# Kernel tuning notes

Hardware: AMD Instinct MI355X
Metric: run time of the kernel (lower is better)

Reference implementation:

```python
import jax, jax.numpy as jnp
import numpy as np

B, N, K = 8, 2048, 30
NF, EF = 128, 128
NPE, NRBF, MAXREL = 16, 16, 32


def _normalize(x, axis=-1, eps=1e-8):
    return x / (jnp.linalg.norm(x, axis=axis, keepdims=True) + eps)


def _gather_nodes(feat, idx):
    # feat [B,N,C], idx [B,N,K] -> [B,N,K,C]
    b = jnp.arange(feat.shape[0])[:, None, None]
    return feat[b, idx]


def _layernorm(x, g, b, eps=1e-5):
    mu = jnp.mean(x, -1, keepdims=True)
    var = jnp.var(x, -1, keepdims=True)
    return (x - mu) * jax.lax.rsqrt(var + eps) * g + b


def _dihedrals(X, eps=1e-7):
    # X [B,N,4,3]; use N,CA,C atoms -> [B,N,6] cos/sin of phi/psi/omega
    Bb, Nn = X.shape[0], X.shape[1]
    Xb = X[:, :, :3, :].reshape(Bb, 3 * Nn, 3)
    U = _normalize(Xb[:, 1:] - Xb[:, :-1])
    u2, u1, u0 = U[:, :-2], U[:, 1:-1], U[:, 2:]
    n2 = _normalize(jnp.cross(u2, u1))
    n1 = _normalize(jnp.cross(u1, u0))
    cosD = jnp.clip(jnp.sum(n2 * n1, -1), -1.0 + eps, 1.0 - eps)
    D = jnp.sign(jnp.sum(u2 * n1, -1)) * jnp.arccos(cosD)
    D = jnp.pad(D, ((0, 0), (1, 2))).reshape(Bb, Nn, 3)
    return jnp.concatenate([jnp.cos(D), jnp.sin(D)], -1)


def _quaternions(R):
    # R [B,N,K,3,3] -> unit quaternion [B,N,K,4]
    Rxx, Ryy, Rzz = R[..., 0, 0], R[..., 1, 1], R[..., 2, 2]
    mag = 0.5 * jnp.sqrt(jnp.abs(1.0 + jnp.stack(
        [Rxx - Ryy - Rzz, -Rxx + Ryy - Rzz, -Rxx - Ryy + Rzz], -1)))
    signs = jnp.sign(jnp.stack(
        [R[..., 2, 1] - R[..., 1, 2], R[..., 0, 2] - R[..., 2, 0], R[..., 1, 0] - R[..., 0, 1]], -1))
    xyz = signs * mag
    w = 0.5 * jnp.sqrt(jax.nn.relu(1.0 + Rxx + Ryy + Rzz))[..., None]
    return _normalize(jnp.concatenate([xyz, w], -1))


def _orientations_coarse(Ca, E_idx):
    # local backbone frames + neighbor direction (3) and relative quaternion (4)
    Bb, Nn = Ca.shape[0], Ca.shape[1]
    U = _normalize(Ca[:, 1:] - Ca[:, :-1])
    u2, u1 = U[:, :-2], U[:, 1:-1]
    n2 = _normalize(jnp.cross(u2, u1))
    o1 = _normalize(u2 - u1)
    O = jnp.stack([o1, n2, jnp.cross(o1, n2)], 2).reshape(Bb, Nn - 3, 9)
    O = jnp.pad(O, ((0, 0), (1, 2), (0, 0)))  # [B,N,9]
    O_nb = _gather_nodes(O, E_idx).reshape(Bb, Nn, -1, 3, 3)
    X_nb = _gather_nodes(Ca, E_idx)
    Of = O.reshape(Bb, Nn, 3, 3)
    dX = X_nb - Ca[:, :, None, :]
    dU = _normalize(jnp.einsum('bnij,bnkj->bnki', Of, dX))
    R = jnp.einsum('bnji,bnkjl->bnkil', Of, O_nb)  # O_i^T @ O_j
    Q = _quaternions(R)
    return jnp.concatenate([dU, Q], -1)  # [B,N,K,7]


def _rbf(D):
    mu = jnp.linspace(2.0, 22.0, NRBF)
    sigma = (22.0 - 2.0) / NRBF
    return jnp.exp(-(((D[..., None] - mu) / sigma) ** 2))


def setup_inputs() -> dict:
    key = jax.random.key(0)
    ks = jax.random.split(key, 8)
    X = jax.random.normal(ks[0], (B, N, 4, 3), dtype=jnp.float32)
    mask = jnp.ones((B, N), dtype=jnp.float32)
    residue_idx = jnp.arange(B * N, dtype=jnp.int32).reshape(B, N)
    chain_labels = jnp.zeros((B, N), dtype=jnp.int32)
    d_pe_in = 2 * MAXREL + 2  # 66
    e_in = NPE + NRBF + 7     # 39
    p = {
        'pe_w': jax.random.normal(ks[1], (d_pe_in, NPE)) / np.sqrt(d_pe_in),
        'pe_b': jnp.zeros((NPE,)),
        'node_l_w': jax.random.normal(ks[2], (6, NF)) / np.sqrt(6.0),
        'node_l_b': jnp.zeros((NF,)),
        'node_emb_w': jax.random.normal(ks[3], (NF, NF)) / np.sqrt(NF),
        'node_emb_b': jnp.zeros((NF,)),
        'edge_l_w': jax.random.normal(ks[4], (e_in, EF)) / np.sqrt(e_in),
        'edge_l_b': jnp.zeros((EF,)),
        'edge_emb_w': jax.random.normal(ks[5], (EF, EF)) / np.sqrt(EF),
        'edge_emb_b': jnp.zeros((EF,)),
        'nn_g': jnp.ones((NF,)), 'nn_b': jnp.zeros((NF,)),
        'ne_g': jnp.ones((EF,)), 'ne_b': jnp.zeros((EF,)),
    }
    return dict(X=X, mask=mask, residue_idx=residue_idx, chain_labels=chain_labels, **p)


def reference(X, mask, residue_idx, chain_labels, pe_w, pe_b, node_l_w, node_l_b,
              node_emb_w, node_emb_b, edge_l_w, edge_l_b, edge_emb_w, edge_emb_b,
              nn_g, nn_b, ne_g, ne_b):
    Ca = X[:, :, 1, :]
    mask2 = mask[:, :, None] * mask[:, None, :]
    D = jnp.sqrt(jnp.sum((Ca[:, :, None] - Ca[:, None, :]) ** 2, -1) + 1e-6)
    D_adj = D + (1.0 - mask2) * 10000.0
    negD, E_idx = jax.lax.top_k(-D_adj, K)  # k nearest
    D_nb = -negD                            # [B,N,K]
    RBF = _rbf(D_nb)                        # [B,N,K,16]
    O_feat = _orientations_coarse(Ca, E_idx)  # [B,N,K,7]
    # positional encodings on gathered residue offsets, masked by chain identity
    offset = residue_idx[:, :, None] - residue_idx[:, None, :]
    off_nb = jnp.take_along_axis(offset, E_idx, axis=2)
    chain_eq = (chain_labels[:, :, None] == chain_labels[:, None, :]).astype(jnp.int32)
    ch_nb = jnp.take_along_axis(chain_eq, E_idx, axis=2)
    d = jnp.clip(off_nb + MAXREL, 0, 2 * MAXREL) * ch_nb + (1 - ch_nb) * (2 * MAXREL + 1)
    d1h = jax.nn.one_hot(d, 2 * MAXREL + 2, dtype=jnp.float32)
    E_pos = d1h @ pe_w + pe_b               # [B,N,K,16]
    V = _dihedrals(X)                       # [B,N,6]
    E = jnp.concatenate([E_pos, RBF, O_feat], -1)  # [B,N,K,39]
    hV = (V @ node_l_w + node_l_b) @ node_emb_w + node_emb_b
    V_out = _layernorm(hV, nn_g, nn_b)
    hE = (E @ edge_l_w + edge_l_b) @ edge_emb_w + edge_emb_b
    E_out = _layernorm(hE, ne_g, ne_b)
    return V_out, E_out, E_idx
```

## Files before the change

kernel.cpp:

```cpp
#include <hip/hip_runtime.h>
#include <hip/hip_bf16.h>
#include <math.h>

#define BB 8
#define NN 2048
#define KK 30
#define NF 128
#define EF 128
#define NPE 16
#define NRBF 16
#define MAXREL 32

#define V_OUT_SZ   (BB*NN*NF)
#define E_OUT_OFF  (V_OUT_SZ)
#define E_OUT_SZ   (BB*NN*KK*EF)
#define EIDX_OUT_OFF (E_OUT_OFF + E_OUT_SZ)

#define WS_EIDX_OFF 0
#define WS_DNB_OFF  1966080
#define WS_O_OFF    3932160
#define WS_V6_OFF   4521984
#define WS_CA4_OFF  4915200
#define WS_W1_OFF   5177344
#define WS_W2_OFF   5193728

typedef __attribute__((ext_vector_type(8))) short bf16x8;
typedef __attribute__((ext_vector_type(4))) float f32x4;
#define MFMA16(a,b,c) __builtin_amdgcn_mfma_f32_16x16x32_bf16(a,b,c,0,0,0)

struct F3 { float x, y, z; };
__device__ inline F3 f3sub(F3 a, F3 b){ return {a.x-b.x, a.y-b.y, a.z-b.z}; }
__device__ inline F3 f3cross(F3 a, F3 b){ return {a.y*b.z - a.z*b.y, a.z*b.x - a.x*b.z, a.x*b.y - a.y*b.x}; }
__device__ inline float f3dot(F3 a, F3 b){ return a.x*b.x + a.y*b.y + a.z*b.z; }
__device__ inline F3 f3norm(F3 v){
    float n = sqrtf(f3dot(v, v));
    float r = 1.0f/(n + 1e-8f);
    return {v.x*r, v.y*r, v.z*r};
}
__device__ inline float sgnf(float x){ return (x>0.f)?1.f:((x<0.f)?-1.f:0.f); }
__device__ inline short f2bf(float f){
    union { __hip_bfloat16 h; short s; } u;
    u.h = __float2bfloat16(f);
    return u.s;
}

template<int CTRL>
__device__ __forceinline__ float fmin_dpp(float x){
    int xi = __float_as_int(x);
    int yi = __builtin_amdgcn_update_dpp(xi, xi, CTRL, 0xf, 0xf, false);
    return fminf(x, __int_as_float(yi));
}
template<int CTRL>
__device__ __forceinline__ unsigned umin_dpp(unsigned x){
    int yi = __builtin_amdgcn_update_dpp((int)x, (int)x, CTRL, 0xf, 0xf, false);
    return min(x, (unsigned)yi);
}

#if __has_builtin(__builtin_amdgcn_permlane16_swap)
__device__ __forceinline__ float fmin_x16(float x){
    unsigned xb = __float_as_uint(x);
    auto r = __builtin_amdgcn_permlane16_swap(xb, xb, false, false);
    return fminf(x, fminf(__uint_as_float(r[0]), __uint_as_float(r[1])));
}
__device__ __forceinline__ unsigned umin_x16(unsigned x){
    auto r = __builtin_amdgcn_permlane16_swap(x, x, false, false);
    return min(x, min((unsigned)r[0], (unsigned)r[1]));
}
#else
__device__ __forceinline__ float fmin_x16(float x){
    int yi = __builtin_amdgcn_ds_swizzle(__float_as_int(x), 0x401F);
    return fminf(x, __int_as_float(yi));
}
__device__ __forceinline__ unsigned umin_x16(unsigned x){
    int yi = __builtin_amdgcn_ds_swizzle((int)x, 0x401F);
    return min(x, (unsigned)yi);
}
#endif

#if __has_builtin(__builtin_amdgcn_permlane32_swap)
__device__ __forceinline__ float fmin_x32(float x){
    unsigned xb = __float_as_uint(x);
    auto r = __builtin_amdgcn_permlane32_swap(xb, xb, false, false);
    return fminf(x, fminf(__uint_as_float(r[0]), __uint_as_float(r[1])));
}
__device__ __forceinline__ unsigned umin_x32(unsigned x){
    auto r = __builtin_amdgcn_permlane32_swap(x, x, false, false);
    return min(x, min((unsigned)r[0], (unsigned)r[1]));
}
#else
__device__ __forceinline__ float fmin_x32(float x){
    return fminf(x, __shfl_xor(x, 32, 64));
}
__device__ __forceinline__ unsigned umin_x32(unsigned x){
    return min(x, (unsigned)__shfl_xor((int)x, 32, 64));
}
#endif

__device__ __forceinline__ float wave_fmin(float x){
    x = fmin_dpp<0xB1>(x);
    x = fmin_dpp<0x4E>(x);
    x = fmin_dpp<0x124>(x);
    x = fmin_dpp<0x128>(x);
    x = fmin_x16(x);
    x = fmin_x32(x);
    return x;
}
__device__ __forceinline__ unsigned wave_umin(unsigned x){
    x = umin_dpp<0xB1>(x);
    x = umin_dpp<0x4E>(x);
    x = umin_dpp<0x124>(x);
    x = umin_dpp<0x128>(x);
    x = umin_x16(x);
    x = umin_x32(x);
    return x;
}

__global__ void prep_kernel(const float* __restrict__ elw,
                            const float* __restrict__ eew,
                            __hip_bfloat16* __restrict__ w1,
                            __hip_bfloat16* __restrict__ w2)
{
    int i = blockIdx.x*256 + threadIdx.x;
    if (i < 8192) {
        int j = i & 7, lane = (i>>3)&63, ks = (i>>9)&1, nf = i>>10;
        int k = ks*32 + (lane>>4)*8 + j;
        int col = nf*16 + (lane&15);
        float v = (k < 39) ? elw[k*128 + col] : 0.f;
        w1[i] = __float2bfloat16(v);
    } else if (i < 8192 + 16384) {
        int i2 = i - 8192;
        int j = i2 & 7, lane = (i2>>3)&63, ks = (i2>>9)&3, nf = i2>>11;
        int k = ks*32 + (lane>>4)*8 + j;
        int col = nf*16 + (lane&15);
        w2[i2] = __float2bfloat16(eew[k*128 + col]);
    }
}

__global__ void geom_kernel(const float* __restrict__ X,
                            const float* __restrict__ mask,
                            float* __restrict__ wsO, float* __restrict__ wsV6,
                            float4* __restrict__ wsCa4)
{
    int ng = blockIdx.x * blockDim.x + threadIdx.x;
    if (ng >= BB*NN) return;
    int b = ng / NN, n = ng % NN;
    const float* Xb = X + (size_t)b * NN * 12;

    {
        const float* cp = X + (size_t)ng*12 + 3;
        wsCa4[ng] = make_float4(cp[0], cp[1], cp[2], mask[ng]);
    }

    int k0 = 3*n - 1;
    F3 P[6];
    #pragma unroll
    for (int t = 0; t < 6; ++t) {
        int m = k0 + t;
        if (m < 0) m = 0;
        if (m > 3*NN-1) m = 3*NN-1;
        int r = m / 3, a = m % 3;
        const float* p = Xb + ((size_t)r*4 + a)*3;
        P[t] = {p[0], p[1], p[2]};
    }
    F3 U[5];
    #pragma unroll
    for (int t = 0; t < 5; ++t) U[t] = f3norm(f3sub(P[t+1], P[t]));

    float Dang[3];
    #pragma unroll
    for (int t = 0; t < 3; ++t) {
        int k = k0 + t;
        if (k < 0 || k > 3*NN-4) { Dang[t] = 0.f; continue; }
        F3 u2 = U[t], u1 = U[t+1], u0 = U[t+2];
        F3 n2 = f3norm(f3cross(u2, u1));
        F3 n1 = f3norm(f3cross(u1, u0));
        float cosD = f3dot(n2, n1);
        cosD = fminf(fmaxf(cosD, -1.f + 1e-7f), 1.f - 1e-7f);
        float s = f3dot(u2, n1);
        Dang[t] = sgnf(s) * acosf(cosD);
    }
    float* v6 = wsV6 + (size_t)ng * 6;
    v6[0] = cosf(Dang[0]); v6[1] = cosf(Dang[1]); v6[2] = cosf(Dang[2]);
    v6[3] = sinf(Dang[0]); v6[4] = sinf(Dang[1]); v6[5] = sinf(Dang[2]);

    float* o = wsO + (size_t)ng * 9;
    if (n >= 1 && n <= NN-3) {
        const float* cb = X + (size_t)b * NN * 12 + 3;
        F3 c0 = {cb[(size_t)(n-1)*12+0], cb[(size_t)(n-1)*12+1], cb[(size_t)(n-1)*12+2]};
        F3 c1 = {cb[(size_t)(n  )*12+0], cb[(size_t)(n  )*12+1], cb[(size_t)(n  )*12+2]};
        F3 c2 = {cb[(size_t)(n+1)*12+0], cb[(size_t)(n+1)*12+1], cb[(size_t)(n+1)*12+2]};
        F3 u2 = f3norm(f3sub(c1, c0));
        F3 u1 = f3norm(f3sub(c2, c1));
        F3 n2 = f3norm(f3cross(u2, u1));
        F3 o1 = f3norm(f3sub(u2, u1));
        F3 r2 = f3cross(o1, n2);
        o[0]=o1.x; o[1]=o1.y; o[2]=o1.z;
        o[3]=n2.x; o[4]=n2.y; o[5]=n2.z;
        o[6]=r2.x; o[7]=r2.y; o[8]=r2.z;
    } else {
        #pragma unroll
        for (int m = 0; m < 9; ++m) o[m] = 0.f;
    }
}

#define KEMPTY 8.9884656743115795e+307

__device__ __forceinline__ double make_key(float d, int j){
    unsigned long long k =
        ((unsigned long long)__float_as_uint(d) << 32) | (unsigned)j;
    return __longlong_as_double((long long)k);
}

__device__ __forceinline__ void ins3(double& q0, double& q1, double& q2, double k){
    double k2 = fmin(k, q2);
    double t1 = fmin(q1, k2); q2 = fmax(q1, k2);
    double t0 = fmin(q0, t1); q1 = fmax(q0, t1);
    q0 = t0;
}

__global__ __launch_bounds__(256, 4) void topk_kernel(
    const float4* __restrict__ wsCa4,
    int* __restrict__ wsEidx, float* __restrict__ wsDnb,
    float* __restrict__ outEidxF)
{
    const int wave = threadIdx.x >> 6, lane = threadIdx.x & 63;
    const int row = blockIdx.x*4 + wave;
    const int b = row >> 11, i = row & (NN-1);

    const float4* cb = wsCa4 + ((size_t)b << 11);
    float4 ci = cb[i];
    float mi = ci.w;

    float dloc[32];
    double q0 = KEMPTY, q1 = KEMPTY, q2 = KEMPTY;
    #pragma unroll
    for (int s = 0; s < 32; ++s) {
        int j = s*64 + lane;
        float4 cj = cb[j];
        float dx = __fsub_rn(ci.x, cj.x);
        float dy = __fsub_rn(ci.y, cj.y);
        float dz = __fsub_rn(ci.z, cj.z);
        float d2 = __fadd_rn(__fadd_rn(__fadd_rn(__fmul_rn(dx,dx),
                                                 __fmul_rn(dy,dy)),
                                       __fmul_rn(dz,dz)), 1e-6f);
        float d = sqrtf(d2);
        d = __fadd_rn(d, __fmul_rn(__fsub_rn(1.0f, __fmul_rn(mi, cj.w)), 10000.0f));
        dloc[s] = d;
        ins3(q0, q1, q2, make_key(d, j));
    }

    double res = KEMPTY;
    #pragma unroll 1
    for (int k = 0; k < KK; ++k) {
        unsigned long long q0b = (unsigned long long)__double_as_longlong(q0);
        float    hd = __uint_as_float((unsigned)(q0b >> 32));
        unsigned hj = (unsigned)q0b;

        float dmin = wave_fmin(hd);
        unsigned cand = (hd == dmin) ? hj : 0xFFFFFFFFu;
        unsigned jmin = wave_umin(cand);

        if (lane == k)
            res = __longlong_as_double((long long)(
                ((unsigned long long)__float_as_uint(dmin) << 32) | jmin));

        if (hd == dmin && hj == jmin) {
            q0 = q1; q1 = q2; q2 = KEMPTY;
            if (__double_as_longlong(q0) == __double_as_longlong(KEMPTY)) {
                double g = __longlong_as_double((long long)(
                    ((unsigned long long)__float_as_uint(dmin) << 32) | jmin));
                #pragma unroll
                for (int s = 0; s < 32; ++s) {
                    double kk = make_key(dloc[s], s*64 + lane);
                    if (!(kk > g)) kk = KEMPTY;
                    ins3(q0, q1, q2, kk);
                }
            }
        }
    }

    if (lane < KK) {
        const size_t rb = (size_t)row * KK;
        unsigned long long gk = (unsigned long long)__double_as_longlong(res);
        int j = (int)(unsigned)gk;
        float dwin = __uint_as_float((unsigned)(gk >> 32));
        wsEidx[rb + lane] = j;
        wsDnb[rb + lane]  = dwin;
        outEidxF[rb + lane] = (float)j;
    }
}

__global__ __launch_bounds__(128) void node_kernel(
    const float* __restrict__ wsV6,
    const float* __restrict__ nlw, const float* __restrict__ nlb,
    const float* __restrict__ new_, const float* __restrict__ neb,
    const float* __restrict__ nng, const float* __restrict__ nnb,
    float* __restrict__ outV)
{
    int f = threadIdx.x;
    __shared__ float h1[128];
    __shared__ float red[2][2];

    float w2[128];
    #pragma unroll
    for (int c = 0; c < 128; ++c) w2[c] = new_[c*128 + f];
    float w1[6];
    #pragma unroll
    for (int c = 0; c < 6; ++c) w1[c] = nlw[c*128 + f];
    float b1v = nlb[f], b2v = neb[f], gv = nng[f], bv = nnb[f];

    for (int gi = 0; gi < 8; ++gi) {
        int row = blockIdx.x*8 + gi;
        float acc = b1v;
        #pragma unroll
        for (int c = 0; c < 6; ++c) acc = fmaf(wsV6[(size_t)row*6 + c], w1[c], acc);
        h1[f] = acc;
        __syncthreads();

        float a2 = b2v;
        #pragma unroll
        for (int c4 = 0; c4 < 32; ++c4) {
            float4 v = *(const float4*)&h1[c4*4];
            a2 = fmaf(v.x, w2[c4*4+0], a2);
            a2 = fmaf(v.y, w2[c4*4+1], a2);
            a2 = fmaf(v.z, w2[c4*4+2], a2);
            a2 = fmaf(v.w, w2[c4*4+3], a2);
        }
        float s = a2, ss = a2*a2;
        #pragma unroll
        for (int off = 32; off; off >>= 1) {
            s  += __shfl_xor(s,  off, 64);
            ss += __shfl_xor(ss, off, 64);
        }
        int wig = f >> 6;
        if ((f & 63) == 0) { red[wig][0] = s; red[wig][1] = ss; }
        __syncthreads();
        float S = red[0][0] + red[1][0], SS = red[0][1] + red[1][1];
        float mu = S * (1.f/128.f);
        float var = SS * (1.f/128.f) - mu*mu;
        float inv = rsqrtf(var + 1e-5f);
        outV[(size_t)row*128 + f] = (a2 - mu)*inv*gv + bv;
        __syncthreads();
    }
}

__global__ __launch_bounds__(256, 4) void edge_mfma_kernel(
    const float4* __restrict__ wsCa4,
    const int* __restrict__ ridx, const int* __restrict__ chain,
    const int* __restrict__ wsEidx, const float* __restrict__ wsDnb,
    const float* __restrict__ wsO,
    const float* __restrict__ pe_w, const float* __restrict__ pe_b,
    const __hip_bfloat16* __restrict__ wsW1, const __hip_bfloat16* __restrict__ wsW2,
    const float* __restrict__ elb, const float* __restrict__ eeb,
    const float* __restrict__ lng, const float* __restrict__ lnb,
    float* __restrict__ outE)
{
    __shared__ char smem[64*72*2 + 64*136*2];
    short* Ef  = (short*)smem;
    short* h1t = (short*)(smem + 64*72*2);
    float* redS  = (float*)smem;
    float* redSS = (float*)(smem + 512);

    const int tid  = threadIdx.x;
    const int wave = tid >> 6, lane = tid & 63;
    const int wm = wave >> 1, wn = wave & 1;
    const int lr = lane & 15, lk = lane >> 4;

    float b1v[4], b2v[4], gv[4], bv[4];
    #pragma unroll
    for (int nf = 0; nf < 4; ++nf) {
        int col = wn*64 + nf*16 + lr;
        b1v[nf] = elb[col]; b2v[nf] = eeb[col];
        gv[nf]  = lng[col]; bv[nf]  = lnb[col];
    }

    for (int idx = tid; idx < 64*25; idx += 256) {
        int r = idx / 25, c = 39 + idx % 25;
        Ef[r*72 + c] = 0;
    }

    const int E0 = blockIdx.x * 64;

    if (wave == 0) {
        int ge = E0 + lane;
        int row = ge / KK;
        int b = row >> 11;
        int j = wsEidx[ge];
        float oi[9], oj[9];
        #pragma unroll
        for (int m = 0; m < 9; ++m) {
            oi[m] = wsO[(size_t)row*9 + m];
            oj[m] = wsO[((size_t)(b*NN) + j)*9 + m];
        }
        float4 ci = wsCa4[row];
        float4 cj = wsCa4[(size_t)b*NN + j];
        float dx = cj.x-ci.x, dy = cj.y-ci.y, dz = cj.z-ci.z;
        float t0 = oi[0]*dx + oi[1]*dy + oi[2]*dz;
        float t1 = oi[3]*dx + oi[4]*dy + oi[5]*dz;
        float t2 = oi[6]*dx + oi[7]*dy + oi[8]*dz;
        float nr = sqrtf(t0*t0 + t1*t1 + t2*t2);
        float iv = 1.f/(nr + 1e-8f);
        short* ef = &Ef[lane*72];
        ef[32] = f2bf(t0*iv); ef[33] = f2bf(t1*iv); ef[34] = f2bf(t2*iv);
        float R00 = oi[0]*oj[0]+oi[3]*oj[3]+oi[6]*oj[6];
        float R01 = oi[0]*oj[1]+oi[3]*oj[4]+oi[6]*oj[7];
        float R02 = oi[0]*oj[2]+oi[3]*oj[5]+oi[6]*oj[8];
        float R10 = oi[1]*oj[0]+oi[4]*oj[3]+oi[7]*oj[6];
        float R11 = oi[1]*oj[1]+oi[4]*oj[4]+oi[7]*oj[7];
        float R12 = oi[1]*oj[2]+oi[4]*oj[5]+oi[7]*oj[8];
        float R20 = oi[2]*oj[0]+oi[5]*oj[3]+oi[8]*oj[6];
        float R21 = oi[2]*oj[1]+oi[5]*oj[4]+oi[8]*oj[7];
        float R22 = oi[2]*oj[2]+oi[5]*oj[5]+oi[8]*oj[8];
        float mx = 0.5f*sqrtf(fabsf(1.f + R00 - R11 - R22));
        float my = 0.5f*sqrtf(fabsf(1.f - R00 + R11 - R22));
        float mz = 0.5f*sqrtf(fabsf(1.f - R00 - R11 + R22));
        float qx = sgnf(R21 - R12)*mx;
        float qy = sgnf(R02 - R20)*my;
        float qz = sgnf(R10 - R01)*mz;
        float qw = 0.5f*sqrtf(fmaxf(0.f, 1.f + R00 + R11 + R22));
        float qn = sqrtf(qx*qx + qy*qy + qz*qz + qw*qw);
        float qi = 1.f/(qn + 1e-8f);
        ef[35] = f2bf(qx*qi); ef[36] = f2bf(qy*qi);
        ef[37] = f2bf(qz*qi); ef[38] = f2bf(qw*qi);
    } else if (wave == 1) {
        int ge = E0 + lane;
        float dnb = wsDnb[ge];
        short* ef = &Ef[lane*72 + 16];
        #pragma unroll
        for (int m = 0; m < 16; ++m) {
            float mu = 2.f + (20.f/15.f)*(float)m;
            float z = (dnb - mu) * 0.8f;
            ef[m] = f2bf(expf(-z*z));
        }
    } else if (wave == 2) {
        int ge = E0 + lane;
        int row = ge / KK;
        int b = row >> 11;
        int j = wsEidx[ge];
        int ri = ridx[row], rj = ridx[b*NN + j];
        int ch = (chain[row] == chain[b*NN + j]) ? 1 : 0;
        int dd = min(max(ri - rj + MAXREL, 0), 2*MAXREL);
        dd = ch ? dd : (2*MAXREL + 1);
        short* ef = &Ef[lane*72];
        #pragma unroll
        for (int m = 0; m < 16; ++m) ef[m] = f2bf(pe_w[dd*16 + m] + pe_b[m]);
    }
    __syncthreads();

    const bf16x8* W1f = (const bf16x8*)wsW1;
    const bf16x8* W2f = (const bf16x8*)wsW2;

    f32x4 acc[2][4];
    #pragma unroll
    for (int mf = 0; mf < 2; ++mf)
        #pragma unroll
        for (int nf = 0; nf < 4; ++nf)
            acc[mf][nf] = (f32x4){0.f, 0.f, 0.f, 0.f};
    #pragma unroll
    for (int ks = 0; ks < 2; ++ks) {
        bf16x8 a0 = *(const bf16x8*)&Ef[(wm*32      + lr)*72 + ks*32 + lk*8];
        bf16x8 a1 = *(const bf16x8*)&Ef[(wm*32 + 16 + lr)*72 + ks*32 + lk*8];
        #pragma unroll
        for (int nf = 0; nf < 4; ++nf) {
            bf16x8 Bf = W1f[((wn*4 + nf)*2 + ks)*64 + lane];
            acc[0][nf] = MFMA16(a0, Bf, acc[0][nf]);
            acc[1][nf] = MFMA16(a1, Bf, acc[1][nf]);
        }
    }
    #pragma unroll
    for (int mf = 0; mf < 2; ++mf)
        #pragma unroll
        for (int nf = 0; nf < 4; ++nf)
            #pragma unroll
            for (int r = 0; r < 4; ++r) {
                int row = wm*32 + mf*16 + lk*4 + r;
                int col = wn*64 + nf*16 + lr;
                h1t[row*136 + col] = f2bf(acc[mf][nf][r] + b1v[nf]);
            }
    __syncthreads();

    f32x4 acc2[2][4];
    #pragma unroll
    for (int mf = 0; mf < 2; ++mf)
        #pragma unroll
        for (int nf = 0; nf < 4; ++nf)
            acc2[mf][nf] = (f32x4){0.f, 0.f, 0.f, 0.f};
    #pragma unroll
    for (int ks = 0; ks < 4; ++ks) {
        bf16x8 a0 = *(const bf16x8*)&h1t[(wm*32      + lr)*136 + ks*32 + lk*8];
        bf16x8 a1 = *(const bf16x8*)&h1t[(wm*32 + 16 + lr)*136 + ks*32 + lk*8];
        #pragma unroll
        for (int nf = 0; nf < 4; ++nf) {
            bf16x8 Bf = W2f[((wn*4 + nf)*4 + ks)*64 + lane];
            acc2[0][nf] = MFMA16(a0, Bf, acc2[0][nf]);
            acc2[1][nf] = MFMA16(a1, Bf, acc2[1][nf]);
        }
    }
    #pragma unroll
    for (int mf = 0; mf < 2; ++mf)
        #pragma unroll
        for (int nf = 0; nf < 4; ++nf)
            #pragma unroll
            for (int r = 0; r < 4; ++r)
                acc2[mf][nf][r] += b2v[nf];

    #pragma unroll
    for (int mf = 0; mf < 2; ++mf) {
        #pragma unroll
        for (int r = 0; r < 4; ++r) {
            float v0 = acc2[mf][0][r], v1 = acc2[mf][1][r];
            float v2 = acc2[mf][2][r], v3 = acc2[mf][3][r];
            float s = v0 + v1 + v2 + v3;
            float q = v0*v0 + v1*v1 + v2*v2 + v3*v3;
            #pragma unroll
            for (int off = 1; off < 16; off <<= 1) {
                s += __shfl_xor(s, off, 64);
                q += __shfl_xor(q, off, 64);
            }
            if (lr == 0) {
                int row = wm*32 + mf*16 + lk*4 + r;
                redS[row*2 + wn] = s; redSS[row*2 + wn] = q;
            }
        }
    }
    __syncthreads();

    const size_t obase = (size_t)E0 * 128;
    #pragma unroll
    for (int mf = 0; mf < 2; ++mf) {
        #pragma unroll
        for (int r = 0; r < 4; ++r) {
            int row = wm*32 + mf*16 + lk*4 + r;
            float S = redS[row*2 + 0] + redS[row*2 + 1];
            float Q = redSS[row*2 + 0] + redSS[row*2 + 1];
            float mu = S * (1.f/128.f);
            float var = Q * (1.f/128.f) - mu*mu;
            float inv = rsqrtf(var + 1e-5f);
            #pragma unroll
            for (int nf = 0; nf < 4; ++nf) {
                int col = wn*64 + nf*16 + lr;
                outE[obase + (size_t)row*128 + col] =
                    (acc2[mf][nf][r] - mu)*inv*gv[nf] + bv[nf];
            }
        }
    }
}

extern "C" void kernel_launch(void* const* d_in, const int* in_sizes, int n_in,
                              void* d_out, int out_size, void* d_ws, size_t ws_size,
                              hipStream_t stream)
{
    const float* X     = (const float*)d_in[0];
    const float* mask  = (const float*)d_in[1];
    const int*   ridx  = (const int*)  d_in[2];
    const int*   chain = (const int*)  d_in[3];
    const float* pe_w  = (const float*)d_in[4];
    const float* pe_b  = (const float*)d_in[5];
    const float* nlw   = (const float*)d_in[6];
    const float* nlb   = (const float*)d_in[7];
    const float* new_  = (const float*)d_in[8];
    const float* neb   = (const float*)d_in[9];
    const float* elw   = (const float*)d_in[10];
    const float* elb   = (const float*)d_in[11];
    const float* eew   = (const float*)d_in[12];
    const float* eeb   = (const float*)d_in[13];
    const float* nng   = (const float*)d_in[14];
    const float* nnb   = (const float*)d_in[15];
    const float* neg_  = (const float*)d_in[16];
    const float* neb_  = (const float*)d_in[17];

    float* out = (float*)d_out;
    char*  ws  = (char*)d_ws;
    int*    wsEidx = (int*)   (ws + WS_EIDX_OFF);
    float*  wsDnb  = (float*) (ws + WS_DNB_OFF);
    float*  wsO    = (float*) (ws + WS_O_OFF);
    float*  wsV6   = (float*) (ws + WS_V6_OFF);
    float4* wsCa4  = (float4*)(ws + WS_CA4_OFF);
    __hip_bfloat16* wsW1 = (__hip_bfloat16*)(ws + WS_W1_OFF);
    __hip_bfloat16* wsW2 = (__hip_bfloat16*)(ws + WS_W2_OFF);

    prep_kernel<<<96, 256, 0, stream>>>(elw, eew, wsW1, wsW2);
    geom_kernel<<<(BB*NN + 255)/256, 256, 0, stream>>>(X, mask, wsO, wsV6, wsCa4);
    topk_kernel<<<BB*NN/4, 256, 0, stream>>>(wsCa4, wsEidx, wsDnb, out + EIDX_OUT_OFF);
    node_kernel<<<BB*NN/8, 128, 0, stream>>>(wsV6, nlw, nlb, new_, neb, nng, nnb, out);
    edge_mfma_kernel<<<BB*NN*KK/64, 256, 0, stream>>>(wsCa4, ridx, chain, wsEidx, wsDnb, wsO,
                                                      pe_w, pe_b, wsW1, wsW2,
                                                      elb, eeb, neg_, neb_, out + E_OUT_OFF);
}
```

Before: 173.6 us.

## Process two top-k rows per wave using half-wave reductions

The top-k kernel now assigns one query row to each 32-lane half of a wave instead of a whole wave. Each lane covers 64 candidates instead of 32, and the cross-32 permlane step is dropped from the min reductions. The aim is to halve the number of serial selection iterations per row and cut reduction latency. In exchange, each lane holds twice as many candidate distances in registers (64 floats), which may lower occupancy under the 256,4 launch bounds, and the per-lane 3-deep queue refills more often.

```diff
diff --git a/kernel.cpp b/kernel.cpp
--- a/kernel.cpp
+++ b/kernel.cpp
@@ -77,41 +77,20 @@
 }
 #endif
 
-#if __has_builtin(__builtin_amdgcn_permlane32_swap)
-__device__ __forceinline__ float fmin_x32(float x){
-    unsigned xb = __float_as_uint(x);
-    auto r = __builtin_amdgcn_permlane32_swap(xb, xb, false, false);
-    return fminf(x, fminf(__uint_as_float(r[0]), __uint_as_float(r[1])));
-}
-__device__ __forceinline__ unsigned umin_x32(unsigned x){
-    auto r = __builtin_amdgcn_permlane32_swap(x, x, false, false);
-    return min(x, min((unsigned)r[0], (unsigned)r[1]));
-}
-#else
-__device__ __forceinline__ float fmin_x32(float x){
-    return fminf(x, __shfl_xor(x, 32, 64));
-}
-__device__ __forceinline__ unsigned umin_x32(unsigned x){
-    return min(x, (unsigned)__shfl_xor((int)x, 32, 64));
-}
-#endif
-
-__device__ __forceinline__ float wave_fmin(float x){
+__device__ __forceinline__ float half_fmin(float x){
     x = fmin_dpp<0xB1>(x);
     x = fmin_dpp<0x4E>(x);
     x = fmin_dpp<0x124>(x);
     x = fmin_dpp<0x128>(x);
     x = fmin_x16(x);
-    x = fmin_x32(x);
     return x;
 }
-__device__ __forceinline__ unsigned wave_umin(unsigned x){
+__device__ __forceinline__ unsigned half_umin(unsigned x){
     x = umin_dpp<0xB1>(x);
     x = umin_dpp<0x4E>(x);
     x = umin_dpp<0x124>(x);
     x = umin_dpp<0x128>(x);
     x = umin_x16(x);
-    x = umin_x32(x);
     return x;
 }
 
@@ -218,33 +197,36 @@
     q0 = t0;
 }
 
+__device__ __forceinline__ float dist_rn(float4 ci, float4 cj){
+    float dx = __fsub_rn(ci.x, cj.x);
+    float dy = __fsub_rn(ci.y, cj.y);
+    float dz = __fsub_rn(ci.z, cj.z);
+    float d2 = __fadd_rn(__fadd_rn(__fadd_rn(__fmul_rn(dx,dx),
+                                             __fmul_rn(dy,dy)),
+                                   __fmul_rn(dz,dz)), 1e-6f);
+    float d = sqrtf(d2);
+    return __fadd_rn(d, __fmul_rn(__fsub_rn(1.0f, __fmul_rn(ci.w, cj.w)), 10000.0f));
+}
+
 __global__ __launch_bounds__(256, 4) void topk_kernel(
     const float4* __restrict__ wsCa4,
     int* __restrict__ wsEidx, float* __restrict__ wsDnb,
     float* __restrict__ outEidxF)
 {
     const int wave = threadIdx.x >> 6, lane = threadIdx.x & 63;
-    const int row = blockIdx.x*4 + wave;
+    const int half = lane >> 5, l = lane & 31;
+    const int row = blockIdx.x*8 + wave*2 + half;
     const int b = row >> 11, i = row & (NN-1);
 
     const float4* cb = wsCa4 + ((size_t)b << 11);
-    float4 ci = cb[i];
-    float mi = ci.w;
-
-    float dloc[32];
+    const float4 ci = cb[i];
+
+    float dloc[64];
     double q0 = KEMPTY, q1 = KEMPTY, q2 = KEMPTY;
     #pragma unroll
-    for (int s = 0; s < 32; ++s) {
-        int j = s*64 + lane;
-        float4 cj = cb[j];
-        float dx = __fsub_rn(ci.x, cj.x);
-        float dy = __fsub_rn(ci.y, cj.y);
-        float dz = __fsub_rn(ci.z, cj.z);
-        float d2 = __fadd_rn(__fadd_rn(__fadd_rn(__fmul_rn(dx,dx),
-                                                 __fmul_rn(dy,dy)),
-                                       __fmul_rn(dz,dz)), 1e-6f);
-        float d = sqrtf(d2);
-        d = __fadd_rn(d, __fmul_rn(__fsub_rn(1.0f, __fmul_rn(mi, cj.w)), 10000.0f));
+    for (int s = 0; s < 64; ++s) {
+        int j = s*32 + l;
+        float d = dist_rn(ci, cb[j]);
         dloc[s] = d;
         ins3(q0, q1, q2, make_key(d, j));
     }
@@ -256,11 +238,11 @@
         float    hd = __uint_as_float((unsigned)(q0b >> 32));
         unsigned hj = (unsigned)q0b;
 
-        float dmin = wave_fmin(hd);
+        float dmin = half_fmin(hd);
         unsigned cand = (hd == dmin) ? hj : 0xFFFFFFFFu;
-        unsigned jmin = wave_umin(cand);
-
-        if (lane == k)
+        unsigned jmin = half_umin(cand);
+
+        if (l == k)
             res = __longlong_as_double((long long)(
                 ((unsigned long long)__float_as_uint(dmin) << 32) | jmin));
 
@@ -270,8 +252,8 @@
                 double g = __longlong_as_double((long long)(
                     ((unsigned long long)__float_as_uint(dmin) << 32) | jmin));
                 #pragma unroll
-                for (int s = 0; s < 32; ++s) {
-                    double kk = make_key(dloc[s], s*64 + lane);
+                for (int s = 0; s < 64; ++s) {
+                    double kk = make_key(dloc[s], s*32 + l);
                     if (!(kk > g)) kk = KEMPTY;
                     ins3(q0, q1, q2, kk);
                 }
@@ -279,14 +261,14 @@
         }
     }
 
-    if (lane < KK) {
+    if (l < KK) {
         const size_t rb = (size_t)row * KK;
         unsigned long long gk = (unsigned long long)__double_as_longlong(res);
         int j = (int)(unsigned)gk;
         float dwin = __uint_as_float((unsigned)(gk >> 32));
-        wsEidx[rb + lane] = j;
-        wsDnb[rb + lane]  = dwin;
-        outEidxF[rb + lane] = (float)j;
+        wsEidx[rb + l] = j;
+        wsDnb[rb + l]  = dwin;
+        outEidxF[rb + l] = (float)j;
     }
 }
 
@@ -581,7 +563,7 @@
 
     prep_kernel<<<96, 256, 0, stream>>>(elw, eew, wsW1, wsW2);
     geom_kernel<<<(BB*NN + 255)/256, 256, 0, stream>>>(X, mask, wsO, wsV6, wsCa4);
-    topk_kernel<<<BB*NN/4, 256, 0, stream>>>(wsCa4, wsEidx, wsDnb, out + EIDX_OUT_OFF);
+    topk_kernel<<<BB*NN/8, 256, 0, stream>>>(wsCa4, wsEidx, wsDnb, out + EIDX_OUT_OFF);
     node_kernel<<<BB*NN/8, 128, 0, stream>>>(wsV6, nlw, nlb, new_, neb, nng, nnb, out);
     edge_mfma_kernel<<<BB*NN*KK/64, 256, 0, stream>>>(wsCa4, ridx, chain, wsEidx, wsDnb, wsO,
                                                       pe_w, pe_b, wsW1, wsW2,
```

Result: slower. 236.9 us (+36.5%).
